# Kernel tuning notes

Hardware: AMD Instinct MI355X
Metric: run time of the kernel (lower is better)

Reference implementation:

```python
import jax, jax.numpy as jnp
import numpy as np

B, N, D = 16, 8192, 64
M, S = 256, 32          # npoints, nsample
OUT = 128
RADIUS = 0.4
WC = 64                 # WeightNet output channels
BN_EPS = 1e-5
_BN_SCALE = 1.0 / np.sqrt(1.0 + BN_EPS)  # eval-mode BN, running mean 0 / var 1


def _bn(x, gamma, beta):
    shp = [1] * x.ndim
    shp[1] = -1
    return gamma.reshape(shp) * (x * _BN_SCALE) + beta.reshape(shp)


def _pdist2(a, b):
    # a (B,P,3), b (B,Q,3) -> (B,P,Q) squared distances
    return (jnp.sum(a * a, -1)[:, :, None] + jnp.sum(b * b, -1)[:, None, :]
            - 2.0 * jnp.einsum('bpd,bqd->bpq', a, b))


def _fps(xyz, npoints):
    # furthest point sampling, pointnet2 semantics (start at index 0)
    Bq, Nq, _ = xyz.shape
    first = jnp.zeros((Bq,), jnp.int32)

    def step(carry, _):
        dist, last = carry
        pt = xyz[jnp.arange(Bq), last]                   # (B,3)
        d = jnp.sum((xyz - pt[:, None, :]) ** 2, -1)
        dist = jnp.minimum(dist, d)
        nxt = jnp.argmax(dist, -1).astype(jnp.int32)
        return (dist, nxt), nxt

    init = (jnp.full((Bq, Nq), 1e10, xyz.dtype), first)
    _, rest = jax.lax.scan(step, init, None, length=npoints - 1)
    return jnp.concatenate([first[None], rest], 0).T     # (B, npoints)


def _ball_query(xyz, new_xyz, radius, nsample):
    # first `nsample` indices within radius, pad by repeating first valid index
    d2 = _pdist2(new_xyz, xyz)                           # (B,M,N)
    n = xyz.shape[1]
    key = jnp.where(d2 <= radius * radius, n - jnp.arange(n, dtype=jnp.int32), 0)
    vals, idx = jax.lax.top_k(key, nsample)              # lowest in-radius indices first
    return jnp.where(vals > 0, idx, idx[:, :, :1])


def _group(x_ch, idx):
    # x_ch (B,C,N), idx (B,M,S) -> (B,C,M,S)
    return jax.vmap(lambda f, i: f[:, i])(x_ch, idx)


def setup_inputs():
    key = jax.random.key(0)
    ks = jax.random.split(key, 8)
    f = jnp.float32

    def w(k, o, i):
        return (jax.random.normal(k, (o, i), f) / np.sqrt(i)).astype(f)

    return {
        'xyz': jax.random.uniform(ks[0], (B, N, 3), f),
        'feature': jax.random.normal(ks[1], (B, D, N), f),
        'w0': w(ks[2], WC, 3), 'b0': jnp.zeros((WC,), f), 'gamma0': jnp.ones((WC,), f), 'beta0': jnp.zeros((WC,), f),
        'w1': w(ks[3], WC, WC), 'b1': jnp.zeros((WC,), f), 'gamma1': jnp.ones((WC,), f), 'beta1': jnp.zeros((WC,), f),
        'w2': w(ks[4], WC, WC), 'b2': jnp.zeros((WC,), f),
        'wl': w(ks[5], OUT, D * WC), 'bl': jnp.zeros((OUT,), f), 'gammal': jnp.ones((OUT,), f), 'betal': jnp.zeros((OUT,), f),
        'wf': w(ks[6], OUT, D + OUT), 'bf': jnp.zeros((OUT,), f), 'gammaf': jnp.ones((OUT,), f), 'betaf': jnp.zeros((OUT,), f),
    }


def reference(xyz, feature, w0, b0, gamma0, beta0, w1, b1, gamma1, beta1, w2, b2,
              wl, bl, gammal, betal, wf, bf, gammaf, betaf):
    relu = jax.nn.relu
    # ---- furthest point sampling ----
    fidx = _fps(xyz, M)                                  # (B,M)
    new_xyz = xyz[jnp.arange(B)[:, None], fidx]          # (B,M,3)
    # ---- ball query + grouping ----
    gidx = _ball_query(xyz, new_xyz, RADIUS, S)          # (B,M,S)
    xyz_ch = jnp.transpose(xyz, (0, 2, 1))               # (B,3,N)
    grouped_xyz = _group(xyz_ch, gidx) - jnp.transpose(new_xyz, (0, 2, 1))[:, :, :, None]  # (B,3,M,S) centered
    grouped_feat = _group(feature, gidx)                 # (B,D,M,S)
    # ---- WeightNet (1x1 convs on offsets) ----
    h = relu(_bn(jnp.einsum('oc,bcms->boms', w0, grouped_xyz) + b0[None, :, None, None], gamma0, beta0))
    h = relu(_bn(jnp.einsum('oc,bcms->boms', w1, h) + b1[None, :, None, None], gamma1, beta1))
    weights = jnp.einsum('oc,bcms->boms', w2, h) + b2[None, :, None, None]  # (B,WC,M,S)
    # ---- weighted aggregation: (B,M,D,S) @ (B,M,S,WC) -> (B,M,D*WC) ----
    agg = jnp.einsum('bdms,bwms->bmdw', grouped_feat, weights).reshape(B, M, D * WC)
    new_feature = relu(_bn(jnp.einsum('od,bmd->bom', wl, agg) + bl[None, :, None], gammal, betal))  # (B,OUT,M)
    # ---- three-NN interpolation back to N points ----
    d2 = _pdist2(xyz, new_xyz)                           # (B,N,M)
    negd, nidx = jax.lax.top_k(-d2, 3)                   # 3 nearest sampled centers
    rd = 1.0 / (-negd + 1e-8)                            # reverse density on squared distance
    wts = rd / jnp.sum(rd, -1, keepdims=True)            # (B,N,3)
    gathered = jax.vmap(lambda f2, i: f2[:, i])(new_feature, nidx)  # (B,OUT,N,3)
    interp = jnp.einsum('bcnk,bnk->bcn', gathered, wts)  # (B,OUT,N)
    # ---- concat skip + final 1x1 conv ----
    cat = jnp.concatenate([interp, feature], 1)          # (B,OUT+D,N)
    return relu(_bn(jnp.einsum('oc,bcn->bon', wf, cat) + bf[None, :, None], gammaf, betaf))
```

## Files before the change

### kernel.cpp

```cpp
#include <hip/hip_runtime.h>
#include <hip/hip_bf16.h>
#include <cstdint>
#include <cstddef>

#define BB   16
#define NN   8192
#define DD   64
#define MM   256
#define SS   32
#define OUTC 128
#define WCC  64

using short8 = __attribute__((ext_vector_type(8))) short;
using f32x4  = __attribute__((ext_vector_type(4))) float;

__device__ __forceinline__ float bnf(float x, float g, float be){
    const float BNS = 0.99999500003749969f;
    return g * (x * BNS) + be;
}
__device__ __forceinline__ unsigned short f2bf(float f){
    __hip_bfloat16 h = __float2bfloat16(f);
    return *reinterpret_cast<unsigned short*>(&h);
}

__global__ __launch_bounds__(256) void k_tf(const float* __restrict__ f, float* __restrict__ fT){
  const int blk = blockIdx.x;
  const int b  = blk >> 7;
  const int n0 = (blk & 127) << 6;
  __shared__ float tile[64][65];
  const int t = threadIdx.x;
  {
    const int d = t >> 2, j0 = (t & 3) << 4;
    const float* src = f + ((size_t)b*DD + d)*NN + n0 + j0;
#pragma unroll
    for (int i=0;i<16;i+=4){
      float4 v = *(const float4*)(src + i);
      tile[d][j0+i+0]=v.x; tile[d][j0+i+1]=v.y; tile[d][j0+i+2]=v.z; tile[d][j0+i+3]=v.w;
    }
  }
  __syncthreads();
  {
    const int j = t >> 2, d0 = (t & 3) << 4;
    float* dst = fT + ((size_t)b*NN + n0 + j)*DD + d0;
#pragma unroll
    for (int i=0;i<16;i+=4){
      float4 v = make_float4(tile[d0+i][j], tile[d0+i+1][j], tile[d0+i+2][j], tile[d0+i+3][j]);
      *(float4*)(dst + i) = v;
    }
  }
}

__global__ __launch_bounds__(256) void k_twl(const float* __restrict__ wl, unsigned short* __restrict__ wlB){
  int idx = (blockIdx.x*256 + threadIdx.x)*4;
  float4 v = *(const float4*)(wl + idx);
  ushort4 h = make_ushort4(f2bf(v.x), f2bf(v.y), f2bf(v.z), f2bf(v.w));
  *(ushort4*)(wlB + idx) = h;
}
__global__ __launch_bounds__(256) void k_twf(const float* __restrict__ wf, float* __restrict__ wfT){
  int idx = blockIdx.x*256 + threadIdx.x;
  if (idx < 192*OUTC){
    int k = idx >> 7, o = idx & 127;
    wfT[idx] = wf[o*192 + k];
  }
}

__global__ __launch_bounds__(512) void k_fps(const float* __restrict__ xyz,
                                             float* __restrict__ nxyz){
  const int b = blockIdx.x;
  const int t = threadIdx.x;
  const float* xb = xyz + (size_t)b*NN*3;
  __shared__ float sxyz[NN*3];
  __shared__ float snew[MM*3];
  __shared__ unsigned long long skey[2][8];
  for (int i = t; i < NN*3; i += 512) sxyz[i] = xb[i];
  float px[16], py[16], pz[16], dist[16];
#pragma unroll
  for (int i=0;i<16;i++){
    int id = i*512 + t;
    px[i] = xb[id*3+0]; py[i] = xb[id*3+1]; pz[i] = xb[id*3+2];
    dist[i] = 1e10f;
  }
  __syncthreads();
  float lx = sxyz[0], ly = sxyz[1], lz = sxyz[2];
  if (t==0){ snew[0]=lx; snew[1]=ly; snew[2]=lz; }
  for (int step=1; step<MM; ++step){
    float bv = 0.0f; int bi = NN-1;
#pragma unroll
    for (int i=0;i<16;i++){
      float dx=px[i]-lx, dy=py[i]-ly, dz=pz[i]-lz;
      float d = dx*dx + dy*dy + dz*dz;
      float nd = fminf(dist[i], d);
      dist[i] = nd;
      bool gt = nd > bv;
      bv = gt ? nd : bv;
      bi = gt ? (i*512 + t) : bi;
    }
    unsigned long long key = ((unsigned long long)__float_as_uint(bv) << 32) | (unsigned)(NN-1 - bi);
#pragma unroll
    for (int off=1; off<64; off<<=1){
      unsigned long long ok = __shfl_xor(key, off, 64);
      if (ok > key) key = ok;
    }
    const int p = step & 1;
    if ((t & 63) == 0) skey[p][t>>6] = key;
    __syncthreads();
    unsigned long long k0=skey[p][0], k1=skey[p][1], k2=skey[p][2], k3=skey[p][3];
    unsigned long long k4=skey[p][4], k5=skey[p][5], k6=skey[p][6], k7=skey[p][7];
    unsigned long long ka = k0>k1?k0:k1, kb2 = k2>k3?k2:k3;
    unsigned long long kc = k4>k5?k4:k5, kd = k6>k7?k6:k7;
    unsigned long long ke = ka>kb2?ka:kb2, kf = kc>kd?kc:kd;
    unsigned long long kw = ke>kf?ke:kf;
    const int bid = (NN-1) - (int)(unsigned)(kw & 0xFFFFFFFFull);
    lx = sxyz[bid*3+0]; ly = sxyz[bid*3+1]; lz = sxyz[bid*3+2];
    if (t==0){ snew[step*3+0]=lx; snew[step*3+1]=ly; snew[step*3+2]=lz; }
  }
  __syncthreads();
  for (int i = t; i < MM*3; i += 512) nxyz[(size_t)b*MM*3 + i] = snew[i];
}

__global__ __launch_bounds__(64) void k_bq_mlp(const float* __restrict__ xyz,
    const float* __restrict__ nxyz,
    const float* __restrict__ w0, const float* __restrict__ b0,
    const float* __restrict__ g0, const float* __restrict__ be0,
    const float* __restrict__ w1, const float* __restrict__ b1,
    const float* __restrict__ g1, const float* __restrict__ be1,
    const float* __restrict__ w2, const float* __restrict__ b2,
    int* __restrict__ gidx, float* __restrict__ wbuf){
  const int bm = blockIdx.x;
  const int b  = bm >> 8;
  const int c  = threadIdx.x;
  __shared__ int   sidx[SS];
  __shared__ float sgx[3][SS];
  __shared__ float sh0[SS][WCC];
  __shared__ float sh1[SS][WCC];

  const float w0r0 = w0[c*3+0], w0r1 = w0[c*3+1], w0r2 = w0[c*3+2];
  const float b0c=b0[c], g0c=g0[c], be0c=be0[c];
  const float b1c=b1[c], g1c=g1[c], be1c=be1[c], b2c=b2[c];
  float w1r[64], w2r[64];
#pragma unroll
  for (int i=0;i<16;i++){
    float4 v = *(const float4*)(w1 + c*64 + i*4);
    w1r[i*4+0]=v.x; w1r[i*4+1]=v.y; w1r[i*4+2]=v.z; w1r[i*4+3]=v.w;
    float4 u = *(const float4*)(w2 + c*64 + i*4);
    w2r[i*4+0]=u.x; w2r[i*4+1]=u.y; w2r[i*4+2]=u.z; w2r[i*4+3]=u.w;
  }
  const float cx = nxyz[bm*3+0], cy = nxyz[bm*3+1], cz = nxyz[bm*3+2];
  const float* xb = xyz + (size_t)b*NN*3;
  const float R2 = (float)(0.4*0.4);
  int cnt = 0;
  for (int n0=0; n0<NN && cnt<SS; n0+=64){
    int n = n0 + c;
    float dx = xb[n*3+0]-cx, dy = xb[n*3+1]-cy, dz = xb[n*3+2]-cz;
    float d2 = dx*dx+dy*dy+dz*dz;
    bool in = (d2 <= R2);
    unsigned long long mk = __ballot(in);
    int rank = cnt + (int)__popcll(mk & ((1ull<<c)-1ull));
    if (in && rank < SS) sidx[rank] = n;
    cnt += (int)__popcll(mk);
  }
  int total = min(cnt, SS);
  __syncthreads();
  int i0 = sidx[0];
  if (c >= total && c < SS) sidx[c] = i0;
  __syncthreads();
  if (c < SS){
    int p = sidx[c];
    gidx[bm*SS + c] = p;
    sgx[0][c] = xb[p*3+0]-cx;
    sgx[1][c] = xb[p*3+1]-cy;
    sgx[2][c] = xb[p*3+2]-cz;
  }
  __syncthreads();
  for (int s=0;s<SS;s++){
    float pre = w0r0*sgx[0][s] + w0r1*sgx[1][s] + w0r2*sgx[2][s] + b0c;
    sh0[s][c] = fmaxf(bnf(pre, g0c, be0c), 0.f);
  }
  __syncthreads();
  for (int s=0;s<SS;s++){
    float a = b1c;
#pragma unroll
    for (int k=0;k<64;k+=4){
      float4 h = *(const float4*)(&sh0[s][k]);
      a += w1r[k]*h.x + w1r[k+1]*h.y + w1r[k+2]*h.z + w1r[k+3]*h.w;
    }
    sh1[s][c] = fmaxf(bnf(a, g1c, be1c), 0.f);
  }
  __syncthreads();
  float* wb = wbuf + (size_t)bm*SS*WCC;
  for (int s=0;s<SS;s++){
    float a = b2c;
#pragma unroll
    for (int k=0;k<64;k+=4){
      float4 h = *(const float4*)(&sh1[s][k]);
      a += w2r[k]*h.x + w2r[k+1]*h.y + w2r[k+2]*h.z + w2r[k+3]*h.w;
    }
    wb[s*WCC + c] = a;
  }
}

__global__ __launch_bounds__(256) void k_agg(const float* __restrict__ featT,
                                             const float* __restrict__ wbuf,
                                             const int* __restrict__ gidx,
                                             unsigned short* __restrict__ aggB){
  const int bm = blockIdx.x;
  const int b  = bm >> 8;
  __shared__ float wt[SS][WCC];
  __shared__ int   sidx[SS];
  const int t = threadIdx.x;
  const float* wsrc = wbuf + (size_t)bm*SS*WCC;
#pragma unroll
  for (int i=0;i<8;i++){
    int li = t + i*256;
    ((float*)wt)[li] = wsrc[li];
  }
  if (t < SS) sidx[t] = gidx[bm*SS + t];
  __syncthreads();
  const int d  = t & 63;
  const int wg = t >> 6;
  float acc[16];
#pragma unroll
  for (int j=0;j<16;j++) acc[j]=0.f;
  const float* fb = featT + (size_t)b*NN*DD;
  for (int s=0;s<SS;s++){
    float fv = fb[(size_t)sidx[s]*DD + d];
#pragma unroll
    for (int j=0;j<16;j++) acc[j] += fv * wt[s][wg*16+j];
  }
  unsigned short h[16];
#pragma unroll
  for (int j=0;j<16;j++) h[j] = f2bf(acc[j]);
  unsigned short* ab = aggB + (size_t)bm*4096 + d*64 + wg*16;
  *(uint4*)(ab)     = *(uint4*)(&h[0]);
  *(uint4*)(ab + 8) = *(uint4*)(&h[8]);
}

__global__ __launch_bounds__(256) void k_nf_part(const unsigned short* __restrict__ aggB,
                                                 const unsigned short* __restrict__ wlB,
                                                 float* __restrict__ part){
  const int blk = blockIdx.x;
  const int rb  = blk >> 2;
  const int ks  = blk & 3;
  const int wid = threadIdx.x >> 6, lane = threadIdx.x & 63;
  const int m0 = rb*64 + wid*16;
  const int r  = lane & 15, kg = lane >> 4;
  f32x4 acc[8];
#pragma unroll
  for (int i=0;i<8;i++) acc[i] = (f32x4){0.f,0.f,0.f,0.f};
  const short* arow = (const short*)aggB + (size_t)(m0 + r)*4096 + ks*1024 + kg*8;
  const short* brow = (const short*)wlB  + (size_t)r*4096        + ks*1024 + kg*8;
#pragma unroll 4
  for (int kc=0; kc<32; kc++){
    short8 a = *(const short8*)(arow + kc*32);
#pragma unroll
    for (int ot=0; ot<8; ot++){
      short8 bfr = *(const short8*)(brow + (size_t)ot*16*4096 + kc*32);
      acc[ot] = __builtin_amdgcn_mfma_f32_16x16x32_bf16(a, bfr, acc[ot], 0, 0, 0);
    }
  }
  float* pb = part + ((size_t)ks << 19);
#pragma unroll
  for (int ot=0; ot<8; ot++){
#pragma unroll
    for (int rr=0; rr<4; rr++){
      int row = m0 + kg*4 + rr;
      pb[(size_t)row*128 + ot*16 + r] = acc[ot][rr];
    }
  }
}

__global__ __launch_bounds__(256) void k_nf_ep(const float* __restrict__ part,
    const float* __restrict__ bl, const float* __restrict__ gl, const float* __restrict__ bel,
    float* __restrict__ nfT){
  const int gid = blockIdx.x*256 + threadIdx.x;
  const int base = gid*4;
  const int o0 = base & 127;
  float4 s0 = *(const float4*)(part + base);
  float4 s1 = *(const float4*)(part + (1<<19) + base);
  float4 s2 = *(const float4*)(part + (2<<19) + base);
  float4 s3 = *(const float4*)(part + (3<<19) + base);
  float sum[4] = {s0.x+s1.x+s2.x+s3.x, s0.y+s1.y+s2.y+s3.y,
                  s0.z+s1.z+s2.z+s3.z, s0.w+s1.w+s2.w+s3.w};
  float ov[4];
#pragma unroll
  for (int j=0;j<4;j++){
    const int o = o0 + j;
    ov[j] = fmaxf(bnf(sum[j] + bl[o], gl[o], bel[o]), 0.f);
  }
  *(float4*)(nfT + base) = make_float4(ov[0],ov[1],ov[2],ov[3]);
}

__global__ __launch_bounds__(256) void k_final(const float* __restrict__ xyz,
    const float* __restrict__ nxyz, const float* __restrict__ nfT,
    const float* __restrict__ feature, const float* __restrict__ wfT,
    const float* __restrict__ bf, const float* __restrict__ gf, const float* __restrict__ bef,
    float* __restrict__ out){
  const int blk = blockIdx.x;
  const int b  = blk >> 6;
  const int n0 = (blk & 63) << 7;
  __shared__ float Wsh[32][128];
  __shared__ float Csh[32][132];
  __shared__ float snew[MM*3];
  __shared__ float sw[128][3];
  __shared__ int   si[128][3];
  const int t = threadIdx.x;
  if (t < 192){
    float4 v = *(const float4*)(nxyz + (size_t)b*MM*3 + t*4);
    snew[t*4+0]=v.x; snew[t*4+1]=v.y; snew[t*4+2]=v.z; snew[t*4+3]=v.w;
  }
  __syncthreads();
  if (t < 128){
    const int n = n0 + t;
    const float x = xyz[((size_t)b*NN+n)*3+0];
    const float y = xyz[((size_t)b*NN+n)*3+1];
    const float z = xyz[((size_t)b*NN+n)*3+2];
    float d1=1e30f, d2=1e30f, d3=1e30f; int i1=0,i2=0,i3=0;
    for (int m=0;m<MM;m++){
      float dx=x-snew[m*3+0], dy=y-snew[m*3+1], dz=z-snew[m*3+2];
      float d = dx*dx+dy*dy+dz*dz;
      if (d < d3){
        if (d < d1){ d3=d2;i3=i2; d2=d1;i2=i1; d1=d;i1=m; }
        else if (d < d2){ d3=d2;i3=i2; d2=d;i2=m; }
        else { d3=d;i3=m; }
      }
    }
    float r1=1.f/(d1+1e-8f), r2=1.f/(d2+1e-8f), r3=1.f/(d3+1e-8f);
    float rs = 1.f/(r1+r2+r3);
    sw[t][0]=r1*rs; sw[t][1]=r2*rs; sw[t][2]=r3*rs;
    si[t][0]=i1; si[t][1]=i2; si[t][2]=i3;
  }
  __syncthreads();

  float acc[8][8];
#pragma unroll
  for (int i=0;i<8;i++)
#pragma unroll
    for (int j=0;j<8;j++) acc[i][j]=0.f;
  const int og = t >> 4, ng = t & 15;
  const float* nfb = nfT + (size_t)b*MM*128;
  for (int k0=0; k0<192; k0+=32){
    {
      const int kk = t >> 3, o0 = (t & 7) << 4;
#pragma unroll
      for (int i=0;i<16;i+=4)
        *(float4*)(&Wsh[kk][o0+i]) = *(const float4*)(wfT + (size_t)(k0+kk)*128 + o0 + i);
    }
    if (k0 < 128){
      const int nn = t >> 1, kb0 = (t & 1) << 4;
      const float w0v = sw[nn][0], w1v = sw[nn][1], w2v = sw[nn][2];
      const float* p0 = nfb + (size_t)si[nn][0]*128 + k0 + kb0;
      const float* p1 = nfb + (size_t)si[nn][1]*128 + k0 + kb0;
      const float* p2 = nfb + (size_t)si[nn][2]*128 + k0 + kb0;
#pragma unroll
      for (int i=0;i<16;i+=4){
        float4 a = *(const float4*)(p0+i);
        float4 bq = *(const float4*)(p1+i);
        float4 cq = *(const float4*)(p2+i);
        Csh[kb0+i+0][nn] = w0v*a.x + w1v*bq.x + w2v*cq.x;
        Csh[kb0+i+1][nn] = w0v*a.y + w1v*bq.y + w2v*cq.y;
        Csh[kb0+i+2][nn] = w0v*a.z + w1v*bq.z + w2v*cq.z;
        Csh[kb0+i+3][nn] = w0v*a.w + w1v*bq.w + w2v*cq.w;
      }
    } else {
      const int kk = t >> 3, nb = (t & 7) << 4;
      const float* src = feature + ((size_t)b*DD + (k0-128) + kk)*NN + n0 + nb;
#pragma unroll
      for (int i=0;i<16;i+=4){
        float4 v = *(const float4*)(src+i);
        *(float4*)(&Csh[kk][nb+i]) = v;
      }
    }
    __syncthreads();
#pragma unroll 8
    for (int kk=0;kk<32;kk++){
      float4 a0 = *(float4*)(&Wsh[kk][og*8]);
      float4 a1 = *(float4*)(&Wsh[kk][og*8+4]);
      float av[8] = {a0.x,a0.y,a0.z,a0.w,a1.x,a1.y,a1.z,a1.w};
      float4 c0 = *(float4*)(&Csh[kk][ng*8]);
      float4 c1 = *(float4*)(&Csh[kk][ng*8+4]);
      float cv[8] = {c0.x,c0.y,c0.z,c0.w,c1.x,c1.y,c1.z,c1.w};
#pragma unroll
      for (int i=0;i<8;i++)
#pragma unroll
        for (int j=0;j<8;j++)
          acc[i][j] += av[i]*cv[j];
    }
    __syncthreads();
  }
#pragma unroll
  for (int i=0;i<8;i++){
    const int o = og*8 + i;
    const float bfo = bf[o], gfo = gf[o], befo = bef[o];
    float ov[8];
#pragma unroll
    for (int j=0;j<8;j++) ov[j] = fmaxf(bnf(acc[i][j] + bfo, gfo, befo), 0.f);
    float* dst = out + ((size_t)b*OUTC + o)*NN + n0 + ng*8;
    *(float4*)(dst)   = make_float4(ov[0],ov[1],ov[2],ov[3]);
    *(float4*)(dst+4) = make_float4(ov[4],ov[5],ov[6],ov[7]);
  }
}

extern "C" void kernel_launch(void* const* d_in, const int* in_sizes, int n_in,
                              void* d_out, int out_size, void* d_ws, size_t ws_size,
                              hipStream_t stream){
  const float* xyz     = (const float*)d_in[0];
  const float* feature = (const float*)d_in[1];
  const float* w0  = (const float*)d_in[2];
  const float* b0  = (const float*)d_in[3];
  const float* g0  = (const float*)d_in[4];
  const float* be0 = (const float*)d_in[5];
  const float* w1  = (const float*)d_in[6];
  const float* b1  = (const float*)d_in[7];
  const float* g1  = (const float*)d_in[8];
  const float* be1 = (const float*)d_in[9];
  const float* w2  = (const float*)d_in[10];
  const float* b2  = (const float*)d_in[11];
  const float* wl  = (const float*)d_in[12];
  const float* bl  = (const float*)d_in[13];
  const float* gl  = (const float*)d_in[14];
  const float* bel = (const float*)d_in[15];
  const float* wf  = (const float*)d_in[16];
  const float* bf  = (const float*)d_in[17];
  const float* gf  = (const float*)d_in[18];
  const float* bef = (const float*)d_in[19];
  float* out = (float*)d_out;

  char* ws = (char*)d_ws;
  float*          featT = (float*)(ws + 0);
  float*          wbuf  = (float*)(ws + 33554432);
  float*          part  = (float*)(ws + 33554432);
  unsigned short* aggB  = (unsigned short*)(ws + 67108864);
  unsigned short* wlB   = (unsigned short*)(ws + 134217728);
  float*          wfT   = (float*)(ws + 136314880);
  float*          nxyz  = (float*)(ws + 136429568);
  int*            gidx  = (int*)  (ws + 136478720);
  float*          nfT   = (float*)(ws + 137003008);

  k_tf     <<<2048, 256, 0, stream>>>(feature, featT);
  k_twl    <<<512,  256, 0, stream>>>(wl, wlB);
  k_twf    <<<96,   256, 0, stream>>>(wf, wfT);
  k_fps    <<<BB,   512, 0, stream>>>(xyz, nxyz);
  k_bq_mlp <<<BB*MM, 64, 0, stream>>>(xyz, nxyz, w0,b0,g0,be0, w1,b1,g1,be1, w2,b2, gidx, wbuf);
  k_agg    <<<BB*MM, 256, 0, stream>>>(featT, wbuf, gidx, aggB);
  k_nf_part<<<256,  256, 0, stream>>>(aggB, wlB, part);
  k_nf_ep  <<<512,  256, 0, stream>>>(part, bl, gl, bel, nfT);
  k_final  <<<BB*(NN/128), 256, 0, stream>>>(xyz, nxyz, nfT, feature, wfT, bf, gf, bef, out);
}
```

Measured before the change: 616.2 us.

## Merge preprocessing kernels, store features in bf16, use MFMA for final conv

Four preprocessing kernels (feature transpose, weight conversions, FPS) become one kernel with a block-range dispatch, so FPS overlaps the transpose work and launch overhead drops. FPS now runs with 256 threads and reduces within each wave using DPP. The transposed features are stored as bf16, halving gather traffic in aggregation and the final conv. The final 1x1 conv with interpolation moves from a shared-memory FP32 GEMM to bf16 MFMA with register-built B fragments, at the cost of lower precision and uncoalesced strided output stores.

```diff
diff --git a/kernel.cpp b/kernel.cpp
--- a/kernel.cpp
+++ b/kernel.cpp
@@ -14,6 +14,15 @@
 using short8 = __attribute__((ext_vector_type(8))) short;
 using f32x4  = __attribute__((ext_vector_type(4))) float;
 
+#ifndef __has_builtin
+#define __has_builtin(x) 0
+#endif
+#if __has_builtin(__builtin_amdgcn_update_dpp) && __has_builtin(__builtin_amdgcn_readlane)
+#define USE_DPP 1
+#else
+#define USE_DPP 0
+#endif
+
 __device__ __forceinline__ float bnf(float x, float g, float be){
     const float BNS = 0.99999500003749969f;
     return g * (x * BNS) + be;
@@ -22,100 +31,140 @@
     __hip_bfloat16 h = __float2bfloat16(f);
     return *reinterpret_cast<unsigned short*>(&h);
 }
-
-__global__ __launch_bounds__(256) void k_tf(const float* __restrict__ f, float* __restrict__ fT){
-  const int blk = blockIdx.x;
-  const int b  = blk >> 7;
-  const int n0 = (blk & 127) << 6;
-  __shared__ float tile[64][65];
+__device__ __forceinline__ float bf2f(unsigned short u){
+    return __uint_as_float(((unsigned)u) << 16);
+}
+
+#define PRE_GRID (16 + 2048 + 512 + 24)
+
+__global__ __launch_bounds__(256) void k_pre(const float* __restrict__ xyz, float* __restrict__ nxyz,
+    const float* __restrict__ feature, unsigned short* __restrict__ featB,
+    const float* __restrict__ wl, unsigned short* __restrict__ wlB,
+    const float* __restrict__ wf, unsigned short* __restrict__ wfB){
+  __shared__ union {
+    struct {
+      float sxyz[NN*3];
+      float snew[MM*3];
+      unsigned long long skey[2][4];
+    } f;
+    float tile[64][65];
+  } sm;
   const int t = threadIdx.x;
+  int blk = blockIdx.x;
+
+  if (blk < 16){
+    const int b = blk;
+    const float* xb = xyz + (size_t)b*NN*3;
+    for (int i = t; i < NN*3; i += 256) sm.f.sxyz[i] = xb[i];
+    float px[32], py[32], pz[32], dist[32];
+#pragma unroll
+    for (int i=0;i<32;i++){
+      int id = i*256 + t;
+      px[i] = xb[id*3+0]; py[i] = xb[id*3+1]; pz[i] = xb[id*3+2];
+      dist[i] = 1e10f;
+    }
+    __syncthreads();
+    float lx = sm.f.sxyz[0], ly = sm.f.sxyz[1], lz = sm.f.sxyz[2];
+    if (t==0){ sm.f.snew[0]=lx; sm.f.snew[1]=ly; sm.f.snew[2]=lz; }
+    for (int step=1; step<MM; ++step){
+      float bv = 0.0f; int bi = NN-1;
+#pragma unroll
+      for (int i=0;i<32;i++){
+        float dx=px[i]-lx, dy=py[i]-ly, dz=pz[i]-lz;
+        float d = dx*dx + dy*dy + dz*dz;
+        float nd = fminf(dist[i], d);
+        dist[i] = nd;
+        bool gt = nd > bv;
+        bv = gt ? nd : bv;
+        bi = gt ? (i*256 + t) : bi;
+      }
+      unsigned long long key;
+#if USE_DPP
+      {
+        float v = bv;
+        int s_;
+        s_ = __builtin_amdgcn_update_dpp(__float_as_int(v), __float_as_int(v), 0x111, 0xF, 0xF, 0); v = fmaxf(v, __int_as_float(s_));
+        s_ = __builtin_amdgcn_update_dpp(__float_as_int(v), __float_as_int(v), 0x112, 0xF, 0xF, 0); v = fmaxf(v, __int_as_float(s_));
+        s_ = __builtin_amdgcn_update_dpp(__float_as_int(v), __float_as_int(v), 0x114, 0xF, 0xF, 0); v = fmaxf(v, __int_as_float(s_));
+        s_ = __builtin_amdgcn_update_dpp(__float_as_int(v), __float_as_int(v), 0x118, 0xF, 0xF, 0); v = fmaxf(v, __int_as_float(s_));
+        s_ = __builtin_amdgcn_update_dpp(__float_as_int(v), __float_as_int(v), 0x142, 0xF, 0xF, 0); v = fmaxf(v, __int_as_float(s_));
+        s_ = __builtin_amdgcn_update_dpp(__float_as_int(v), __float_as_int(v), 0x143, 0xF, 0xF, 0); v = fmaxf(v, __int_as_float(s_));
+        float wmax = __int_as_float(__builtin_amdgcn_readlane(__float_as_int(v), 63));
+        unsigned cm = (bv == wmax) ? (unsigned)bi : 0xFFFFFFFFu;
+        unsigned u_;
+        u_ = (unsigned)__builtin_amdgcn_update_dpp((int)cm, (int)cm, 0x111, 0xF, 0xF, 0); cm = cm < u_ ? cm : u_;
+        u_ = (unsigned)__builtin_amdgcn_update_dpp((int)cm, (int)cm, 0x112, 0xF, 0xF, 0); cm = cm < u_ ? cm : u_;
+        u_ = (unsigned)__builtin_amdgcn_update_dpp((int)cm, (int)cm, 0x114, 0xF, 0xF, 0); cm = cm < u_ ? cm : u_;
+        u_ = (unsigned)__builtin_amdgcn_update_dpp((int)cm, (int)cm, 0x118, 0xF, 0xF, 0); cm = cm < u_ ? cm : u_;
+        u_ = (unsigned)__builtin_amdgcn_update_dpp((int)cm, (int)cm, 0x142, 0xF, 0xF, 0); cm = cm < u_ ? cm : u_;
+        u_ = (unsigned)__builtin_amdgcn_update_dpp((int)cm, (int)cm, 0x143, 0xF, 0xF, 0); cm = cm < u_ ? cm : u_;
+        unsigned widx = (unsigned)__builtin_amdgcn_readlane((int)cm, 63);
+        key = ((unsigned long long)__float_as_uint(wmax) << 32) | (unsigned)(NN-1 - widx);
+      }
+#else
+      key = ((unsigned long long)__float_as_uint(bv) << 32) | (unsigned)(NN-1 - bi);
+#pragma unroll
+      for (int off=1; off<64; off<<=1){
+        unsigned long long ok = __shfl_xor(key, off, 64);
+        if (ok > key) key = ok;
+      }
+#endif
+      const int p = step & 1;
+      if ((t & 63) == 0) sm.f.skey[p][t>>6] = key;
+      __syncthreads();
+      unsigned long long k0=sm.f.skey[p][0], k1=sm.f.skey[p][1], k2=sm.f.skey[p][2], k3=sm.f.skey[p][3];
+      unsigned long long ka = k0>k1?k0:k1, kb = k2>k3?k2:k3;
+      unsigned long long kw = ka>kb?ka:kb;
+      const int bid = (NN-1) - (int)(unsigned)(kw & 0xFFFFFFFFull);
+      lx = sm.f.sxyz[bid*3+0]; ly = sm.f.sxyz[bid*3+1]; lz = sm.f.sxyz[bid*3+2];
+      if (t==0){ sm.f.snew[step*3+0]=lx; sm.f.snew[step*3+1]=ly; sm.f.snew[step*3+2]=lz; }
+    }
+    __syncthreads();
+    for (int i = t; i < MM*3; i += 256) nxyz[(size_t)b*MM*3 + i] = sm.f.snew[i];
+    return;
+  }
+  blk -= 16;
+  if (blk < 2048){
+    const int b  = blk >> 7;
+    const int n0 = (blk & 127) << 6;
+    {
+      const int d = t >> 2, j0 = (t & 3) << 4;
+      const float* src = feature + ((size_t)b*DD + d)*NN + n0 + j0;
+#pragma unroll
+      for (int i=0;i<16;i+=4){
+        float4 v = *(const float4*)(src + i);
+        sm.tile[d][j0+i+0]=v.x; sm.tile[d][j0+i+1]=v.y; sm.tile[d][j0+i+2]=v.z; sm.tile[d][j0+i+3]=v.w;
+      }
+    }
+    __syncthreads();
+    {
+      const int j = t >> 2, d0 = (t & 3) << 4;
+      unsigned short hv[16];
+#pragma unroll
+      for (int i=0;i<16;i++) hv[i] = f2bf(sm.tile[d0+i][j]);
+      unsigned short* dst = featB + ((size_t)b*NN + n0 + j)*64 + d0;
+      *(uint4*)(dst)     = *(uint4*)(&hv[0]);
+      *(uint4*)(dst + 8) = *(uint4*)(&hv[8]);
+    }
+    return;
+  }
+  blk -= 2048;
+  if (blk < 512){
+    int idx = (blk*256 + t)*4;
+    float4 v = *(const float4*)(wl + idx);
+    ushort4 h = make_ushort4(f2bf(v.x), f2bf(v.y), f2bf(v.z), f2bf(v.w));
+    *(ushort4*)(wlB + idx) = h;
+    return;
+  }
+  blk -= 512;
   {
-    const int d = t >> 2, j0 = (t & 3) << 4;
-    const float* src = f + ((size_t)b*DD + d)*NN + n0 + j0;
-#pragma unroll
-    for (int i=0;i<16;i+=4){
-      float4 v = *(const float4*)(src + i);
-      tile[d][j0+i+0]=v.x; tile[d][j0+i+1]=v.y; tile[d][j0+i+2]=v.z; tile[d][j0+i+3]=v.w;
-    }
-  }
-  __syncthreads();
-  {
-    const int j = t >> 2, d0 = (t & 3) << 4;
-    float* dst = fT + ((size_t)b*NN + n0 + j)*DD + d0;
-#pragma unroll
-    for (int i=0;i<16;i+=4){
-      float4 v = make_float4(tile[d0+i][j], tile[d0+i+1][j], tile[d0+i+2][j], tile[d0+i+3][j]);
-      *(float4*)(dst + i) = v;
-    }
-  }
-}
-
-__global__ __launch_bounds__(256) void k_twl(const float* __restrict__ wl, unsigned short* __restrict__ wlB){
-  int idx = (blockIdx.x*256 + threadIdx.x)*4;
-  float4 v = *(const float4*)(wl + idx);
-  ushort4 h = make_ushort4(f2bf(v.x), f2bf(v.y), f2bf(v.z), f2bf(v.w));
-  *(ushort4*)(wlB + idx) = h;
-}
-__global__ __launch_bounds__(256) void k_twf(const float* __restrict__ wf, float* __restrict__ wfT){
-  int idx = blockIdx.x*256 + threadIdx.x;
-  if (idx < 192*OUTC){
-    int k = idx >> 7, o = idx & 127;
-    wfT[idx] = wf[o*192 + k];
-  }
-}
-
-__global__ __launch_bounds__(512) void k_fps(const float* __restrict__ xyz,
-                                             float* __restrict__ nxyz){
-  const int b = blockIdx.x;
-  const int t = threadIdx.x;
-  const float* xb = xyz + (size_t)b*NN*3;
-  __shared__ float sxyz[NN*3];
-  __shared__ float snew[MM*3];
-  __shared__ unsigned long long skey[2][8];
-  for (int i = t; i < NN*3; i += 512) sxyz[i] = xb[i];
-  float px[16], py[16], pz[16], dist[16];
-#pragma unroll
-  for (int i=0;i<16;i++){
-    int id = i*512 + t;
-    px[i] = xb[id*3+0]; py[i] = xb[id*3+1]; pz[i] = xb[id*3+2];
-    dist[i] = 1e10f;
-  }
-  __syncthreads();
-  float lx = sxyz[0], ly = sxyz[1], lz = sxyz[2];
-  if (t==0){ snew[0]=lx; snew[1]=ly; snew[2]=lz; }
-  for (int step=1; step<MM; ++step){
-    float bv = 0.0f; int bi = NN-1;
-#pragma unroll
-    for (int i=0;i<16;i++){
-      float dx=px[i]-lx, dy=py[i]-ly, dz=pz[i]-lz;
-      float d = dx*dx + dy*dy + dz*dz;
-      float nd = fminf(dist[i], d);
-      dist[i] = nd;
-      bool gt = nd > bv;
-      bv = gt ? nd : bv;
-      bi = gt ? (i*512 + t) : bi;
-    }
-    unsigned long long key = ((unsigned long long)__float_as_uint(bv) << 32) | (unsigned)(NN-1 - bi);
-#pragma unroll
-    for (int off=1; off<64; off<<=1){
-      unsigned long long ok = __shfl_xor(key, off, 64);
-      if (ok > key) key = ok;
-    }
-    const int p = step & 1;
-    if ((t & 63) == 0) skey[p][t>>6] = key;
-    __syncthreads();
-    unsigned long long k0=skey[p][0], k1=skey[p][1], k2=skey[p][2], k3=skey[p][3];
-    unsigned long long k4=skey[p][4], k5=skey[p][5], k6=skey[p][6], k7=skey[p][7];
-    unsigned long long ka = k0>k1?k0:k1, kb2 = k2>k3?k2:k3;
-    unsigned long long kc = k4>k5?k4:k5, kd = k6>k7?k6:k7;
-    unsigned long long ke = ka>kb2?ka:kb2, kf = kc>kd?kc:kd;
-    unsigned long long kw = ke>kf?ke:kf;
-    const int bid = (NN-1) - (int)(unsigned)(kw & 0xFFFFFFFFull);
-    lx = sxyz[bid*3+0]; ly = sxyz[bid*3+1]; lz = sxyz[bid*3+2];
-    if (t==0){ snew[step*3+0]=lx; snew[step*3+1]=ly; snew[step*3+2]=lz; }
-  }
-  __syncthreads();
-  for (int i = t; i < MM*3; i += 512) nxyz[(size_t)b*MM*3 + i] = snew[i];
+    int idx = (blk*256 + t)*4;
+    if (idx < 128*192){
+      float4 v = *(const float4*)(wf + idx);
+      ushort4 h = make_ushort4(f2bf(v.x), f2bf(v.y), f2bf(v.z), f2bf(v.w));
+      *(ushort4*)(wfB + idx) = h;
+    }
+  }
 }
 
 __global__ __launch_bounds__(64) void k_bq_mlp(const float* __restrict__ xyz,
@@ -199,7 +248,7 @@
   }
 }
 
-__global__ __launch_bounds__(256) void k_agg(const float* __restrict__ featT,
+__global__ __launch_bounds__(256) void k_agg(const unsigned short* __restrict__ featB,
                                              const float* __restrict__ wbuf,
                                              const int* __restrict__ gidx,
                                              unsigned short* __restrict__ aggB){
@@ -221,9 +270,9 @@
   float acc[16];
 #pragma unroll
   for (int j=0;j<16;j++) acc[j]=0.f;
-  const float* fb = featT + (size_t)b*NN*DD;
+  const unsigned short* fb = featB + (size_t)b*NN*64;
   for (int s=0;s<SS;s++){
-    float fv = fb[(size_t)sidx[s]*DD + d];
+    float fv = bf2f(fb[(size_t)sidx[s]*64 + d]);
 #pragma unroll
     for (int j=0;j<16;j++) acc[j] += fv * wt[s][wg*16+j];
   }
@@ -292,14 +341,12 @@
 
 __global__ __launch_bounds__(256) void k_final(const float* __restrict__ xyz,
     const float* __restrict__ nxyz, const float* __restrict__ nfT,
-    const float* __restrict__ feature, const float* __restrict__ wfT,
+    const unsigned short* __restrict__ featB, const unsigned short* __restrict__ wfB,
     const float* __restrict__ bf, const float* __restrict__ gf, const float* __restrict__ bef,
     float* __restrict__ out){
   const int blk = blockIdx.x;
   const int b  = blk >> 6;
   const int n0 = (blk & 63) << 7;
-  __shared__ float Wsh[32][128];
-  __shared__ float Csh[32][132];
   __shared__ float snew[MM*3];
   __shared__ float sw[128][3];
   __shared__ int   si[128][3];
@@ -331,72 +378,76 @@
   }
   __syncthreads();
 
-  float acc[8][8];
-#pragma unroll
-  for (int i=0;i<8;i++)
-#pragma unroll
-    for (int j=0;j<8;j++) acc[i][j]=0.f;
-  const int og = t >> 4, ng = t & 15;
+  const int w = t >> 6, lane = t & 63;
+  const int r = lane & 15, kg = lane >> 4;
+  float wA[8][3]; int iA[8][3];
+#pragma unroll
+  for (int nt=0;nt<8;nt++){
+    int n = nt*16 + r;
+    wA[nt][0]=sw[n][0]; wA[nt][1]=sw[n][1]; wA[nt][2]=sw[n][2];
+    iA[nt][0]=si[n][0]*128; iA[nt][1]=si[n][1]*128; iA[nt][2]=si[n][2]*128;
+  }
   const float* nfb = nfT + (size_t)b*MM*128;
-  for (int k0=0; k0<192; k0+=32){
-    {
-      const int kk = t >> 3, o0 = (t & 7) << 4;
-#pragma unroll
-      for (int i=0;i<16;i+=4)
-        *(float4*)(&Wsh[kk][o0+i]) = *(const float4*)(wfT + (size_t)(k0+kk)*128 + o0 + i);
-    }
-    if (k0 < 128){
-      const int nn = t >> 1, kb0 = (t & 1) << 4;
-      const float w0v = sw[nn][0], w1v = sw[nn][1], w2v = sw[nn][2];
-      const float* p0 = nfb + (size_t)si[nn][0]*128 + k0 + kb0;
-      const float* p1 = nfb + (size_t)si[nn][1]*128 + k0 + kb0;
-      const float* p2 = nfb + (size_t)si[nn][2]*128 + k0 + kb0;
-#pragma unroll
-      for (int i=0;i<16;i+=4){
-        float4 a = *(const float4*)(p0+i);
-        float4 bq = *(const float4*)(p1+i);
-        float4 cq = *(const float4*)(p2+i);
-        Csh[kb0+i+0][nn] = w0v*a.x + w1v*bq.x + w2v*cq.x;
-        Csh[kb0+i+1][nn] = w0v*a.y + w1v*bq.y + w2v*cq.y;
-        Csh[kb0+i+2][nn] = w0v*a.z + w1v*bq.z + w2v*cq.z;
-        Csh[kb0+i+3][nn] = w0v*a.w + w1v*bq.w + w2v*cq.w;
+  const unsigned short* fbB = featB + ((size_t)b*NN + n0)*64;
+  const unsigned short* wfRow0 = wfB + (size_t)(w*32 +      r)*192 + kg*8;
+  const unsigned short* wfRow1 = wfB + (size_t)(w*32 + 16 + r)*192 + kg*8;
+  f32x4 acc[2][8];
+#pragma unroll
+  for (int i=0;i<2;i++)
+#pragma unroll
+    for (int j=0;j<8;j++) acc[i][j] = (f32x4){0.f,0.f,0.f,0.f};
+
+#pragma unroll
+  for (int c=0;c<6;c++){
+    short8 a0 = *(const short8*)(wfRow0 + c*32);
+    short8 a1 = *(const short8*)(wfRow1 + c*32);
+    if (c < 4){
+      const int k8 = c*32 + kg*8;
+#pragma unroll
+      for (int nt=0;nt<8;nt++){
+        const float* p0 = nfb + iA[nt][0] + k8;
+        const float* p1 = nfb + iA[nt][1] + k8;
+        const float* p2 = nfb + iA[nt][2] + k8;
+        float4 xa = *(const float4*)(p0), xb4 = *(const float4*)(p0+4);
+        float4 ya = *(const float4*)(p1), yb4 = *(const float4*)(p1+4);
+        float4 za = *(const float4*)(p2), zb4 = *(const float4*)(p2+4);
+        const float w0v=wA[nt][0], w1v=wA[nt][1], w2v=wA[nt][2];
+        float e0 = w0v*xa.x + w1v*ya.x + w2v*za.x;
+        float e1 = w0v*xa.y + w1v*ya.y + w2v*za.y;
+        float e2 = w0v*xa.z + w1v*ya.z + w2v*za.z;
+        float e3 = w0v*xa.w + w1v*ya.w + w2v*za.w;
+        float e4 = w0v*xb4.x + w1v*yb4.x + w2v*zb4.x;
+        float e5 = w0v*xb4.y + w1v*yb4.y + w2v*zb4.y;
+        float e6 = w0v*xb4.z + w1v*yb4.z + w2v*zb4.z;
+        float e7 = w0v*xb4.w + w1v*yb4.w + w2v*zb4.w;
+        short8 bfr = { (short)f2bf(e0), (short)f2bf(e1), (short)f2bf(e2), (short)f2bf(e3),
+                       (short)f2bf(e4), (short)f2bf(e5), (short)f2bf(e6), (short)f2bf(e7) };
+        acc[0][nt] = __builtin_amdgcn_mfma_f32_16x16x32_bf16(a0, bfr, acc[0][nt], 0, 0, 0);
+        acc[1][nt] = __builtin_amdgcn_mfma_f32_16x16x32_bf16(a1, bfr, acc[1][nt], 0, 0, 0);
       }
     } else {
-      const int kk = t >> 3, nb = (t & 7) << 4;
-      const float* src = feature + ((size_t)b*DD + (k0-128) + kk)*NN + n0 + nb;
-#pragma unroll
-      for (int i=0;i<16;i+=4){
-        float4 v = *(const float4*)(src+i);
-        *(float4*)(&Csh[kk][nb+i]) = v;
-      }
-    }
-    __syncthreads();
-#pragma unroll 8
-    for (int kk=0;kk<32;kk++){
-      float4 a0 = *(float4*)(&Wsh[kk][og*8]);
-      float4 a1 = *(float4*)(&Wsh[kk][og*8+4]);
-      float av[8] = {a0.x,a0.y,a0.z,a0.w,a1.x,a1.y,a1.z,a1.w};
-      float4 c0 = *(float4*)(&Csh[kk][ng*8]);
-      float4 c1 = *(float4*)(&Csh[kk][ng*8+4]);
-      float cv[8] = {c0.x,c0.y,c0.z,c0.w,c1.x,c1.y,c1.z,c1.w};
-#pragma unroll
-      for (int i=0;i<8;i++)
-#pragma unroll
-        for (int j=0;j<8;j++)
-          acc[i][j] += av[i]*cv[j];
-    }
-    __syncthreads();
-  }
-#pragma unroll
-  for (int i=0;i<8;i++){
-    const int o = og*8 + i;
-    const float bfo = bf[o], gfo = gf[o], befo = bef[o];
-    float ov[8];
-#pragma unroll
-    for (int j=0;j<8;j++) ov[j] = fmaxf(bnf(acc[i][j] + bfo, gfo, befo), 0.f);
-    float* dst = out + ((size_t)b*OUTC + o)*NN + n0 + ng*8;
-    *(float4*)(dst)   = make_float4(ov[0],ov[1],ov[2],ov[3]);
-    *(float4*)(dst+4) = make_float4(ov[4],ov[5],ov[6],ov[7]);
+      const int d8 = (c-4)*32 + kg*8;
+#pragma unroll
+      for (int nt=0;nt<8;nt++){
+        short8 bfr = *(const short8*)(fbB + (size_t)(nt*16 + r)*64 + d8);
+        acc[0][nt] = __builtin_amdgcn_mfma_f32_16x16x32_bf16(a0, bfr, acc[0][nt], 0, 0, 0);
+        acc[1][nt] = __builtin_amdgcn_mfma_f32_16x16x32_bf16(a1, bfr, acc[1][nt], 0, 0, 0);
+      }
+    }
+  }
+#pragma unroll
+  for (int ot=0; ot<2; ot++){
+#pragma unroll
+    for (int rr=0; rr<4; rr++){
+      const int o = w*32 + ot*16 + kg*4 + rr;
+      const float bfo = bf[o], gfo = gf[o], befo = bef[o];
+      float* dst = out + ((size_t)b*OUTC + o)*NN + n0 + r;
+#pragma unroll
+      for (int nt=0;nt<8;nt++){
+        float val = fmaxf(bnf(acc[ot][nt][rr] + bfo, gfo, befo), 0.f);
+        dst[nt*16] = val;
+      }
+    }
   }
 }
 
@@ -426,23 +477,20 @@
   float* out = (float*)d_out;
 
   char* ws = (char*)d_ws;
-  float*          featT = (float*)(ws + 0);
-  float*          wbuf  = (float*)(ws + 33554432);
-  float*          part  = (float*)(ws + 33554432);
-  unsigned short* aggB  = (unsigned short*)(ws + 67108864);
-  unsigned short* wlB   = (unsigned short*)(ws + 134217728);
-  float*          wfT   = (float*)(ws + 136314880);
-  float*          nxyz  = (float*)(ws + 136429568);
-  int*            gidx  = (int*)  (ws + 136478720);
-  float*          nfT   = (float*)(ws + 137003008);
-
-  k_tf     <<<2048, 256, 0, stream>>>(feature, featT);
-  k_twl    <<<512,  256, 0, stream>>>(wl, wlB);
-  k_twf    <<<96,   256, 0, stream>>>(wf, wfT);
-  k_fps    <<<BB,   512, 0, stream>>>(xyz, nxyz);
+  unsigned short* featB = (unsigned short*)(ws + 0);
+  float*          wbuf  = (float*)(ws + 16777216);
+  float*          part  = (float*)(ws + 16777216);
+  unsigned short* aggB  = (unsigned short*)(ws + 50331648);
+  unsigned short* wlB   = (unsigned short*)(ws + 83886080);
+  unsigned short* wfB   = (unsigned short*)(ws + 84934656);
+  float*          nxyz  = (float*)(ws + 84983808);
+  int*            gidx  = (int*)  (ws + 85032960);
+  float*          nfT   = (float*)(ws + 85557248);
+
+  k_pre    <<<PRE_GRID, 256, 0, stream>>>(xyz, nxyz, feature, featB, wl, wlB, wf, wfB);
   k_bq_mlp <<<BB*MM, 64, 0, stream>>>(xyz, nxyz, w0,b0,g0,be0, w1,b1,g1,be1, w2,b2, gidx, wbuf);
-  k_agg    <<<BB*MM, 256, 0, stream>>>(featT, wbuf, gidx, aggB);
+  k_agg    <<<BB*MM, 256, 0, stream>>>(featB, wbuf, gidx, aggB);
   k_nf_part<<<256,  256, 0, stream>>>(aggB, wlB, part);
   k_nf_ep  <<<512,  256, 0, stream>>>(part, bl, gl, bel, nfT);
-  k_final  <<<BB*(NN/128), 256, 0, stream>>>(xyz, nxyz, nfT, feature, wfT, bf, gf, bef, out);
-}
+  k_final  <<<BB*(NN/128), 256, 0, stream>>>(xyz, nxyz, nfT, featB, wfB, bf, gf, bef, out);
+}
```

Measured after the change: 592.6 us. 3.8% less time.
